# Kernel optimization log

Measured on AMD Instinct MI355X. Metric: run time of the kernel, lower is better.

Reference implementation:

```python
import jax, jax.numpy as jnp
import numpy as np

B, T, C = 4, 2048, 1024
H = 16  # NUM_HEADS
HD = C // H  # head_dim = 64


def setup_inputs() -> dict:
    key = jax.random.key(0)
    k1, k2, k3 = jax.random.split(key, 3)
    x = jax.random.normal(k1, (B, T, C), dtype=jnp.float32)
    # nn.Linear weights: stored as [out, in]; apply as x @ W.T
    W_attn = jax.random.normal(k2, (3 * C, C), dtype=jnp.float32) * (1.0 / np.sqrt(C))
    W_proj = jax.random.normal(k3, (C, C), dtype=jnp.float32) * (1.0 / np.sqrt(C))
    return {"x": x, "W_attn": W_attn, "W_proj": W_proj}


def reference(x, W_attn, W_proj):
    Bv, Tv, Cv = x.shape
    qkv = x @ W_attn.T  # [B, T, 3C]
    q, k, v = jnp.split(qkv, 3, axis=2)
    # [B, H, T, HD]
    q = q.reshape(Bv, Tv, H, HD).transpose(0, 2, 1, 3)
    k = k.reshape(Bv, Tv, H, HD).transpose(0, 2, 1, 3)
    v = v.reshape(Bv, Tv, H, HD).transpose(0, 2, 1, 3)
    att = jnp.einsum("bhqd,bhkd->bhqk", q, k) * (1.0 / np.sqrt(HD))
    causal = jnp.tril(jnp.ones((Tv, Tv), dtype=bool))
    att = jnp.where(causal[None, None, :, :], att, -jnp.inf)
    att = jax.nn.softmax(att, axis=-1)
    y = jnp.einsum("bhqk,bhkd->bhqd", att, v)
    y = y.transpose(0, 2, 1, 3).reshape(Bv, Tv, Cv)
    return y @ W_proj.T
```

## Files before the change

kernel.cpp:

```cpp
#include <hip/hip_runtime.h>

typedef _Float16 f16;
typedef _Float16 half8 __attribute__((ext_vector_type(8)));
typedef _Float16 half4v __attribute__((ext_vector_type(4)));
typedef __fp16 fp16x2 __attribute__((ext_vector_type(2)));
typedef float floatx4 __attribute__((ext_vector_type(4)));
typedef unsigned int uint;

constexpr int Bsz = 4, Tseq = 2048, Cdim = 1024, NH = 16, HDim = 64;
constexpr int Mtok = Bsz * Tseq;
constexpr int NQT = Tseq / 64;
constexpr float QSCALE = 0.18033688f;

#define GLDS16(src, dst) __builtin_amdgcn_global_load_lds( \
    (const __attribute__((address_space(1))) void*)(src),  \
    (__attribute__((address_space(3))) void*)(dst), 16, 0, 0)

__device__ __forceinline__ float fexp2(float x) { return __builtin_amdgcn_exp2f(x); }
__device__ __forceinline__ uint pkrtz(float a, float b) {
  fp16x2 h = __builtin_amdgcn_cvt_pkrtz(a, b);
  return __builtin_bit_cast(uint, h);
}

__global__ void cvt3_kernel(const float* __restrict__ x, const float* __restrict__ wa,
                            const float* __restrict__ wp,
                            f16* __restrict__ xh, f16* __restrict__ wah, f16* __restrict__ wph) {
  constexpr int nx = Mtok * Cdim, nwa = 3 * Cdim * Cdim, nwp = Cdim * Cdim;
  int i = (blockIdx.x * blockDim.x + threadIdx.x) * 4;
  const float* src; f16* dst; int off;
  if (i < nx)            { src = x;  dst = xh;  off = i; }
  else if (i < nx + nwa) { src = wa; dst = wah; off = i - nx; }
  else                   { src = wp; dst = wph; off = i - nx - nwa; }
  float4 v = *(const float4*)(src + off);
  half4v o;
  o[0] = (f16)v.x; o[1] = (f16)v.y; o[2] = (f16)v.z; o[3] = (f16)v.w;
  *(half4v*)(dst + off) = o;
}

template<int EPI>
__device__ __forceinline__ void gemm_body(f16* As, f16* Bs,
    const f16* __restrict__ X, const f16* __restrict__ W,
    float* __restrict__ outF,
    f16* __restrict__ q_out, f16* __restrict__ k_out, f16* __restrict__ v_out,
    int N, int K, int bid)
{
  constexpr int BK = 32;
  const int tid = threadIdx.x;
  const int wave = tid >> 6;
  const int lane = tid & 63;
  const int g = lane >> 4, lm = lane & 15;
  const int nbn = N / 128;
  const int bm = bid / nbn;
  const int bn = bid % nbn;
  const int m0 = bm * 128, n0 = bn * 128;
  const int wr = wave >> 1, wc = wave & 1;

  floatx4 acc[4][4];
#pragma unroll
  for (int i = 0; i < 4; ++i)
#pragma unroll
    for (int j = 0; j < 4; ++j) acc[i][j] = (floatx4)0.0f;

  for (int k0 = 0; k0 < K; k0 += BK) {
    __syncthreads();
#pragma unroll
    for (int t = 0; t < 2; ++t) {
      int row = (wave * 2 + t) * 16 + (lane >> 2);
      int cg = (lane & 3) ^ ((row >> 1) & 3);
      const f16* srcA = X + (size_t)(m0 + row) * K + k0 + cg * 8;
      GLDS16(srcA, (char*)As + (wave * 2 + t) * 1024);
      const f16* srcB = W + (size_t)(n0 + row) * K + k0 + cg * 8;
      GLDS16(srcB, (char*)Bs + (wave * 2 + t) * 1024);
    }
    __syncthreads();

    half8 af[4], bf[4];
#pragma unroll
    for (int i = 0; i < 4; ++i) {
      int rowa = wr * 64 + i * 16 + lm;
      int cga = g ^ ((rowa >> 1) & 3);
      af[i] = *(const half8*)((const char*)As + rowa * 64 + cga * 16);
      int rowb = wc * 64 + i * 16 + lm;
      int cgb = g ^ ((rowb >> 1) & 3);
      bf[i] = *(const half8*)((const char*)Bs + rowb * 64 + cgb * 16);
    }
#pragma unroll
    for (int i = 0; i < 4; ++i)
#pragma unroll
      for (int j = 0; j < 4; ++j)
        acc[i][j] = __builtin_amdgcn_mfma_f32_16x16x32_f16(af[i], bf[j], acc[i][j], 0, 0, 0);
  }

#pragma unroll
  for (int i = 0; i < 4; ++i) {
#pragma unroll
    for (int j = 0; j < 4; ++j) {
#pragma unroll
      for (int r = 0; r < 4; ++r) {
        int m = m0 + wr * 64 + i * 16 + 4 * g + r;
        int n = n0 + wc * 64 + j * 16 + lm;
        float v = acc[i][j][r];
        if constexpr (EPI == 1) {
          outF[(size_t)m * N + n] = v;
        } else if constexpr (EPI == 0) {
          int which = n >> 10;
          int inner = n & 1023;
          int h = inner >> 6, hd = inner & 63;
          int b = m >> 11, t = m & 2047;
          if (which == 0) {
            v *= QSCALE;
            q_out[(((size_t)(b * NH + h)) * Tseq + t) * HDim + hd] = (f16)v;
          } else {
            k_out[(((size_t)(b * NH + h)) * Tseq + t) * HDim + hd] = (f16)v;
          }
        } else {
          int h = m >> 6, hd = m & 63;
          int b = n >> 11, t = n & 2047;
          v_out[(((size_t)(b * NH + h)) * HDim + hd) * Tseq + t] = (f16)v;
        }
      }
    }
  }
}

__global__ __launch_bounds__(256)
void qkv_kernel(const f16* __restrict__ xh, const f16* __restrict__ wAh,
                f16* __restrict__ Qh, f16* __restrict__ Kh, f16* __restrict__ Vth) {
  __shared__ __align__(16) f16 As[128 * 32];
  __shared__ __align__(16) f16 Bs[128 * 32];
  int sbid = (blockIdx.x & 7) * 192 + (blockIdx.x >> 3);
  if (sbid < 1024)
    gemm_body<0>(As, Bs, xh, wAh, nullptr, Qh, Kh, nullptr, 2048, Cdim, sbid);
  else
    gemm_body<2>(As, Bs, wAh + (size_t)2048 * Cdim, xh, nullptr, nullptr, nullptr, Vth,
                 Mtok, Cdim, sbid - 1024);
}

__global__ __launch_bounds__(256)
void proj_kernel(const f16* __restrict__ yh, const f16* __restrict__ wPh, float* __restrict__ out) {
  __shared__ __align__(16) f16 As[128 * 32];
  __shared__ __align__(16) f16 Bs[128 * 32];
  int sbid = (blockIdx.x & 7) * 64 + (blockIdx.x >> 3);
  gemm_body<1>(As, Bs, yh, wPh, out, nullptr, nullptr, nullptr, Cdim, Cdim, sbid);
}

__device__ __forceinline__ void softmax_tile(floatx4* s, float& l_run,
                                             bool diag, int j0, int qg, char* pwrow, int g, int lm) {
  if (diag) {
#pragma unroll
    for (int nf = 0; nf < 4; ++nf)
#pragma unroll
      for (int r = 0; r < 4; ++r)
        if (j0 + nf * 16 + 4 * g + r > qg) s[nf][r] = -1e30f;
  }
  float rs = 0.f;
#pragma unroll
  for (int nf = 0; nf < 4; ++nf) {
    float p0 = fexp2(s[nf][0]), p1 = fexp2(s[nf][1]);
    float p2 = fexp2(s[nf][2]), p3 = fexp2(s[nf][3]);
    rs += (p0 + p1) + (p2 + p3);
    uint lo = pkrtz(p0, p1), hi = pkrtz(p2, p3);
    int slot = 2 * nf + (g >> 1);
    uint2 u; u.x = lo; u.y = hi;
    *(uint2*)(pwrow + 16 * (slot ^ (lm & 7)) + 8 * (g & 1)) = u;
  }
  l_run += rs;
}

__device__ __forceinline__ void store_o(const floatx4* acc, float l, int q0w, int g, int lm,
                                        f16* __restrict__ Y, int b, int h) {
  l += __shfl_xor(l, 16, 64);
  l += __shfl_xor(l, 32, 64);
#pragma unroll
  for (int r = 0; r < 4; ++r) {
    float lq = __shfl(l, 4 * g + r, 64);
    float inv = 1.0f / lq;
    int t = q0w + 4 * g + r;
    size_t base = ((size_t)(b * Tseq + t)) * Cdim + h * HDim;
#pragma unroll
    for (int ng = 0; ng < 4; ++ng)
      Y[base + ng * 16 + lm] = (f16)(acc[ng][r] * inv);
  }
}

__global__ __launch_bounds__(256)
void attn_kernel(const f16* __restrict__ Q, const f16* __restrict__ Kg,
                 const f16* __restrict__ Vt, f16* __restrict__ Y)
{
  __shared__ __align__(16) char smem[40960];
  int wg = blockIdx.x;
  int lin = (wg & 7) * 128 + (wg >> 3);
  const int p  = lin & 15;
  const int bh = lin >> 4;
  const int itB = NQT - p;
  const f16* Qb  = Q  + (size_t)bh * Tseq * HDim;
  const f16* Kb  = Kg + (size_t)bh * Tseq * HDim;
  const f16* Vtb = Vt + (size_t)bh * HDim * Tseq;

  const int tid = threadIdx.x, w = tid >> 6, lane = tid & 63;
  const int g = lane >> 4, lm = lane & 15;
  char* pwrow = smem + 32768 + w * 2048 + lm * 128;
  const int b = bh >> 4, h = bh & 15;

  int q0 = (NQT - 1 - p) * 64;
  int qg = q0 + w * 16 + lm;
  half8 qf0 = *(const half8*)(Qb + (size_t)(q0 + w * 16 + lm) * HDim + g * 8);
  half8 qf1 = *(const half8*)(Qb + (size_t)(q0 + w * 16 + lm) * HDim + 32 + g * 8);

  floatx4 acc[4];
  float l = 0.f;
#pragma unroll
  for (int ng = 0; ng < 4; ++ng) acc[ng] = (floatx4)0.f;

  const int srow = w * 8 + (lane >> 3);
  const int sslot = lane & 7;

  auto stage = [&](int j0s, int buf) {
#pragma unroll
    for (int t = 0; t < 2; ++t) {
      int row = srow + t * 32;
      int cg = sslot ^ (row & 7);
      GLDS16(Kb + (size_t)(j0s + row) * HDim + cg * 8,
             smem + buf * 8192 + (w * 8 + t * 32) * 128);
      GLDS16(Vtb + (size_t)row * Tseq + j0s + cg * 8,
             smem + 16384 + buf * 8192 + (w * 8 + t * 32) * 128);
    }
  };

  stage(0, 0);

  for (int it = 0; it < NQT + 1; ++it) {
    const bool lastB = (it == itB - 1);
    const bool last  = (it == NQT);
    const int jt = (it < itB) ? it : it - itB;
    const int j0 = jt * 64;

    if (!last) {
      const int itn = it + 1;
      const int jtn = (itn < itB) ? itn : itn - itB;
      stage(jtn * 64, itn & 1);
      asm volatile("s_waitcnt vmcnt(4)" ::: "memory");
    } else {
      asm volatile("s_waitcnt vmcnt(0)" ::: "memory");
    }
    __builtin_amdgcn_s_barrier();

    char* kb   = smem + (it & 1) * 8192;
    char* vbuf = smem + 16384 + (it & 1) * 8192;

    floatx4 s[4];
    __builtin_amdgcn_s_setprio(1);
#pragma unroll
    for (int nf = 0; nf < 4; ++nf) {
      half8 kf0 = *(const half8*)(kb + (nf * 16 + lm) * 128 + 16 * ((g)     ^ (lm & 7)));
      half8 kf1 = *(const half8*)(kb + (nf * 16 + lm) * 128 + 16 * ((4 + g) ^ (lm & 7)));
      s[nf] = __builtin_amdgcn_mfma_f32_16x16x32_f16(kf0, qf0, (floatx4)0.f, 0, 0, 0);
      s[nf] = __builtin_amdgcn_mfma_f32_16x16x32_f16(kf1, qf1, s[nf], 0, 0, 0);
    }
    __builtin_amdgcn_s_setprio(0);

    softmax_tile(s, l, lastB || last, j0, qg, pwrow, g, lm);
    half8 pa0 = *(const half8*)(pwrow + 16 * ((g)     ^ (lm & 7)));
    half8 pa1 = *(const half8*)(pwrow + 16 * ((4 + g) ^ (lm & 7)));

    __builtin_amdgcn_s_setprio(1);
#pragma unroll
    for (int c = 0; c < 2; ++c)
#pragma unroll
      for (int ng = 0; ng < 4; ++ng) {
        half8 vbf = *(const half8*)(vbuf + (ng * 16 + lm) * 128 + 16 * ((4 * c + g) ^ (lm & 7)));
        acc[ng] = __builtin_amdgcn_mfma_f32_16x16x32_f16(c ? pa1 : pa0, vbf, acc[ng], 0, 0, 0);
      }
    __builtin_amdgcn_s_setprio(0);

    __builtin_amdgcn_s_barrier();

    if (lastB) {
      store_o(acc, l, q0 + 16 * w, g, lm, Y, b, h);
      q0 = p * 64;
      qg = q0 + w * 16 + lm;
      qf0 = *(const half8*)(Qb + (size_t)(q0 + w * 16 + lm) * HDim + g * 8);
      qf1 = *(const half8*)(Qb + (size_t)(q0 + w * 16 + lm) * HDim + 32 + g * 8);
      l = 0.f;
#pragma unroll
      for (int ng = 0; ng < 4; ++ng) acc[ng] = (floatx4)0.f;
    }
  }

  store_o(acc, l, q0 + 16 * w, g, lm, Y, b, h);
}

extern "C" void kernel_launch(void* const* d_in, const int* in_sizes, int n_in,
                              void* d_out, int out_size, void* d_ws, size_t ws_size,
                              hipStream_t stream)
{
  const float* x      = (const float*)d_in[0];
  const float* W_attn = (const float*)d_in[1];
  const float* W_proj = (const float*)d_in[2];
  float* out = (float*)d_out;

  char* ws = (char*)d_ws;
  f16* xh  = (f16*)(ws);
  f16* wAh = (f16*)(ws + (size_t)(16u << 20));
  f16* wPh = (f16*)(ws + (size_t)(22u << 20));
  f16* Qh  = (f16*)(ws + (size_t)(24u << 20));
  f16* Kh  = (f16*)(ws + (size_t)(40u << 20));
  f16* Vth = (f16*)(ws + (size_t)(56u << 20));
  f16* yh  = xh;

  constexpr int ntot = (Mtok * Cdim + 3 * Cdim * Cdim + Cdim * Cdim) / 4;
  cvt3_kernel<<<(ntot + 255) / 256, 256, 0, stream>>>(x, W_attn, W_proj, xh, wAh, wPh);

  qkv_kernel<<<dim3(1536), 256, 0, stream>>>(xh, wAh, Qh, Kh, Vth);

  attn_kernel<<<dim3(1024), 256, 0, stream>>>(Qh, Kh, Vth, yh);

  proj_kernel<<<dim3(512), 256, 0, stream>>>(yh, wPh, out);
}
```

Measured before the change: 172.3 us.

## Double-buffer LDS in GEMM body to overlap global loads with MFMA

The shared GEMM used by the QKV and projection kernels now uses two LDS stages. The loads for the next K slice are issued before the MFMAs on the current slice run, and fine-grained vmcnt waits replace the full syncthreads pair. This hides global-to-LDS latency behind compute in both GEMMs. In exchange, LDS per block doubles to 32 KB, which can lower occupancy, and correctness now relies on hand-written waitcnt and barrier ordering.

```diff
diff --git a/kernel.cpp b/kernel.cpp
--- a/kernel.cpp
+++ b/kernel.cpp
@@ -38,7 +38,7 @@
 }
 
 template<int EPI>
-__device__ __forceinline__ void gemm_body(f16* As, f16* Bs,
+__device__ __forceinline__ void gemm_body(char* smem,
     const f16* __restrict__ X, const f16* __restrict__ W,
     float* __restrict__ outF,
     f16* __restrict__ q_out, f16* __restrict__ k_out, f16* __restrict__ v_out,
@@ -55,40 +55,61 @@
   const int m0 = bm * 128, n0 = bn * 128;
   const int wr = wave >> 1, wc = wave & 1;
 
+  const int srow = (lane >> 2);
+  const int scg0 = (lane & 3);
+
+  auto stageAB = [&](int k0, int buf) {
+#pragma unroll
+    for (int t = 0; t < 2; ++t) {
+      int row = (wave * 2 + t) * 16 + srow;
+      int cg = scg0 ^ ((row >> 1) & 3);
+      GLDS16(X + (size_t)(m0 + row) * K + k0 + cg * 8,
+             smem + buf * 16384 + (wave * 2 + t) * 1024);
+      GLDS16(W + (size_t)(n0 + row) * K + k0 + cg * 8,
+             smem + buf * 16384 + 8192 + (wave * 2 + t) * 1024);
+    }
+  };
+
   floatx4 acc[4][4];
 #pragma unroll
   for (int i = 0; i < 4; ++i)
 #pragma unroll
     for (int j = 0; j < 4; ++j) acc[i][j] = (floatx4)0.0f;
 
+  stageAB(0, 0);
+  int cur = 0;
+
   for (int k0 = 0; k0 < K; k0 += BK) {
-    __syncthreads();
-#pragma unroll
-    for (int t = 0; t < 2; ++t) {
-      int row = (wave * 2 + t) * 16 + (lane >> 2);
-      int cg = (lane & 3) ^ ((row >> 1) & 3);
-      const f16* srcA = X + (size_t)(m0 + row) * K + k0 + cg * 8;
-      GLDS16(srcA, (char*)As + (wave * 2 + t) * 1024);
-      const f16* srcB = W + (size_t)(n0 + row) * K + k0 + cg * 8;
-      GLDS16(srcB, (char*)Bs + (wave * 2 + t) * 1024);
-    }
-    __syncthreads();
+    const bool more = (k0 + BK < K);
+    if (more) {
+      stageAB(k0 + BK, cur ^ 1);
+      asm volatile("s_waitcnt vmcnt(4)" ::: "memory");
+    } else {
+      asm volatile("s_waitcnt vmcnt(0)" ::: "memory");
+    }
+    __builtin_amdgcn_s_barrier();
+
+    const char* As = smem + cur * 16384;
+    const char* Bs = smem + cur * 16384 + 8192;
 
     half8 af[4], bf[4];
 #pragma unroll
     for (int i = 0; i < 4; ++i) {
       int rowa = wr * 64 + i * 16 + lm;
       int cga = g ^ ((rowa >> 1) & 3);
-      af[i] = *(const half8*)((const char*)As + rowa * 64 + cga * 16);
+      af[i] = *(const half8*)(As + rowa * 64 + cga * 16);
       int rowb = wc * 64 + i * 16 + lm;
       int cgb = g ^ ((rowb >> 1) & 3);
-      bf[i] = *(const half8*)((const char*)Bs + rowb * 64 + cgb * 16);
+      bf[i] = *(const half8*)(Bs + rowb * 64 + cgb * 16);
     }
 #pragma unroll
     for (int i = 0; i < 4; ++i)
 #pragma unroll
       for (int j = 0; j < 4; ++j)
         acc[i][j] = __builtin_amdgcn_mfma_f32_16x16x32_f16(af[i], bf[j], acc[i][j], 0, 0, 0);
+
+    __builtin_amdgcn_s_barrier();
+    cur ^= 1;
   }
 
 #pragma unroll
@@ -126,22 +147,20 @@
 __global__ __launch_bounds__(256)
 void qkv_kernel(const f16* __restrict__ xh, const f16* __restrict__ wAh,
                 f16* __restrict__ Qh, f16* __restrict__ Kh, f16* __restrict__ Vth) {
-  __shared__ __align__(16) f16 As[128 * 32];
-  __shared__ __align__(16) f16 Bs[128 * 32];
+  __shared__ __align__(16) char smem[32768];
   int sbid = (blockIdx.x & 7) * 192 + (blockIdx.x >> 3);
   if (sbid < 1024)
-    gemm_body<0>(As, Bs, xh, wAh, nullptr, Qh, Kh, nullptr, 2048, Cdim, sbid);
+    gemm_body<0>(smem, xh, wAh, nullptr, Qh, Kh, nullptr, 2048, Cdim, sbid);
   else
-    gemm_body<2>(As, Bs, wAh + (size_t)2048 * Cdim, xh, nullptr, nullptr, nullptr, Vth,
+    gemm_body<2>(smem, wAh + (size_t)2048 * Cdim, xh, nullptr, nullptr, nullptr, Vth,
                  Mtok, Cdim, sbid - 1024);
 }
 
 __global__ __launch_bounds__(256)
 void proj_kernel(const f16* __restrict__ yh, const f16* __restrict__ wPh, float* __restrict__ out) {
-  __shared__ __align__(16) f16 As[128 * 32];
-  __shared__ __align__(16) f16 Bs[128 * 32];
+  __shared__ __align__(16) char smem[32768];
   int sbid = (blockIdx.x & 7) * 64 + (blockIdx.x >> 3);
-  gemm_body<1>(As, Bs, yh, wPh, out, nullptr, nullptr, nullptr, Cdim, Cdim, sbid);
+  gemm_body<1>(smem, yh, wPh, out, nullptr, nullptr, nullptr, Cdim, Cdim, sbid);
 }
 
 __device__ __forceinline__ void softmax_tile(floatx4* s, float& l_run,
```

New measurement: 178.0 us. 1.03x slower.

## Fuse x fp32-to-fp16 conversion into QKV GEMM tile loads

Applied to the files above, without the earlier changes.

The standalone conversion of activation x to fp16 is removed. The QKV GEMM now loads fp32 x tiles directly into LDS with a new XOR swizzle and converts them to half8 when reading fragments, so the fp16 copy of x is never written to or read back from global memory. The cost is twice the LDS footprint for the x operand and twice the global bytes per x tile inside the GEMM, which is re-read across the N tiles, plus extra conversion ALU work in the inner loop.

```diff
diff --git a/kernel.cpp b/kernel.cpp
--- a/kernel.cpp
+++ b/kernel.cpp
@@ -22,29 +22,28 @@
   return __builtin_bit_cast(uint, h);
 }
 
-__global__ void cvt3_kernel(const float* __restrict__ x, const float* __restrict__ wa,
-                            const float* __restrict__ wp,
-                            f16* __restrict__ xh, f16* __restrict__ wah, f16* __restrict__ wph) {
-  constexpr int nx = Mtok * Cdim, nwa = 3 * Cdim * Cdim, nwp = Cdim * Cdim;
+__global__ void cvt2_kernel(const float* __restrict__ wa, const float* __restrict__ wp,
+                            f16* __restrict__ wah, f16* __restrict__ wph) {
+  constexpr int nwa = 3 * Cdim * Cdim;
   int i = (blockIdx.x * blockDim.x + threadIdx.x) * 4;
   const float* src; f16* dst; int off;
-  if (i < nx)            { src = x;  dst = xh;  off = i; }
-  else if (i < nx + nwa) { src = wa; dst = wah; off = i - nx; }
-  else                   { src = wp; dst = wph; off = i - nx - nwa; }
+  if (i < nwa) { src = wa; dst = wah; off = i; }
+  else         { src = wp; dst = wph; off = i - nwa; }
   float4 v = *(const float4*)(src + off);
   half4v o;
   o[0] = (f16)v.x; o[1] = (f16)v.y; o[2] = (f16)v.z; o[3] = (f16)v.w;
   *(half4v*)(dst + off) = o;
 }
 
-template<int EPI>
-__device__ __forceinline__ void gemm_body(f16* As, f16* Bs,
-    const f16* __restrict__ X, const f16* __restrict__ W,
+template<int EPI, int AF32, int BF32>
+__device__ __forceinline__ void gemm_body(char* smem,
+    const void* Aop, const void* Bop,
     float* __restrict__ outF,
     f16* __restrict__ q_out, f16* __restrict__ k_out, f16* __restrict__ v_out,
     int N, int K, int bid)
 {
   constexpr int BK = 32;
+  constexpr int BOFF = AF32 ? 16384 : 8192;
   const int tid = threadIdx.x;
   const int wave = tid >> 6;
   const int lane = tid & 63;
@@ -63,14 +62,43 @@
 
   for (int k0 = 0; k0 < K; k0 += BK) {
     __syncthreads();
-#pragma unroll
-    for (int t = 0; t < 2; ++t) {
-      int row = (wave * 2 + t) * 16 + (lane >> 2);
-      int cg = (lane & 3) ^ ((row >> 1) & 3);
-      const f16* srcA = X + (size_t)(m0 + row) * K + k0 + cg * 8;
-      GLDS16(srcA, (char*)As + (wave * 2 + t) * 1024);
-      const f16* srcB = W + (size_t)(n0 + row) * K + k0 + cg * 8;
-      GLDS16(srcB, (char*)Bs + (wave * 2 + t) * 1024);
+    if constexpr (AF32) {
+      const float* Af = (const float*)Aop;
+#pragma unroll
+      for (int t = 0; t < 4; ++t) {
+        int row = wave * 8 + (lane >> 3) + t * 32;
+        int s = (lane & 7) ^ (row & 7);
+        GLDS16(Af + (size_t)(m0 + row) * K + k0 + s * 4,
+               smem + (wave * 8 + t * 32) * 128);
+      }
+    } else {
+      const f16* Ah = (const f16*)Aop;
+#pragma unroll
+      for (int t = 0; t < 2; ++t) {
+        int row = (wave * 2 + t) * 16 + (lane >> 2);
+        int cg = (lane & 3) ^ ((row >> 1) & 3);
+        GLDS16(Ah + (size_t)(m0 + row) * K + k0 + cg * 8,
+               smem + (wave * 2 + t) * 1024);
+      }
+    }
+    if constexpr (BF32) {
+      const float* Bf = (const float*)Bop;
+#pragma unroll
+      for (int t = 0; t < 4; ++t) {
+        int row = wave * 8 + (lane >> 3) + t * 32;
+        int s = (lane & 7) ^ (row & 7);
+        GLDS16(Bf + (size_t)(n0 + row) * K + k0 + s * 4,
+               smem + BOFF + (wave * 8 + t * 32) * 128);
+      }
+    } else {
+      const f16* Bh = (const f16*)Bop;
+#pragma unroll
+      for (int t = 0; t < 2; ++t) {
+        int row = (wave * 2 + t) * 16 + (lane >> 2);
+        int cg = (lane & 3) ^ ((row >> 1) & 3);
+        GLDS16(Bh + (size_t)(n0 + row) * K + k0 + cg * 8,
+               smem + BOFF + (wave * 2 + t) * 1024);
+      }
     }
     __syncthreads();
 
@@ -78,11 +106,29 @@
 #pragma unroll
     for (int i = 0; i < 4; ++i) {
       int rowa = wr * 64 + i * 16 + lm;
-      int cga = g ^ ((rowa >> 1) & 3);
-      af[i] = *(const half8*)((const char*)As + rowa * 64 + cga * 16);
+      if constexpr (AF32) {
+        float4 f0 = *(const float4*)(smem + rowa * 128 + 16 * ((2 * g)     ^ (rowa & 7)));
+        float4 f1 = *(const float4*)(smem + rowa * 128 + 16 * ((2 * g + 1) ^ (rowa & 7)));
+        half8 v;
+        v[0] = (f16)f0.x; v[1] = (f16)f0.y; v[2] = (f16)f0.z; v[3] = (f16)f0.w;
+        v[4] = (f16)f1.x; v[5] = (f16)f1.y; v[6] = (f16)f1.z; v[7] = (f16)f1.w;
+        af[i] = v;
+      } else {
+        int cga = g ^ ((rowa >> 1) & 3);
+        af[i] = *(const half8*)(smem + rowa * 64 + cga * 16);
+      }
       int rowb = wc * 64 + i * 16 + lm;
-      int cgb = g ^ ((rowb >> 1) & 3);
-      bf[i] = *(const half8*)((const char*)Bs + rowb * 64 + cgb * 16);
+      if constexpr (BF32) {
+        float4 f0 = *(const float4*)(smem + BOFF + rowb * 128 + 16 * ((2 * g)     ^ (rowb & 7)));
+        float4 f1 = *(const float4*)(smem + BOFF + rowb * 128 + 16 * ((2 * g + 1) ^ (rowb & 7)));
+        half8 v;
+        v[0] = (f16)f0.x; v[1] = (f16)f0.y; v[2] = (f16)f0.z; v[3] = (f16)f0.w;
+        v[4] = (f16)f1.x; v[5] = (f16)f1.y; v[6] = (f16)f1.z; v[7] = (f16)f1.w;
+        bf[i] = v;
+      } else {
+        int cgb = g ^ ((rowb >> 1) & 3);
+        bf[i] = *(const half8*)(smem + BOFF + rowb * 64 + cgb * 16);
+      }
     }
 #pragma unroll
     for (int i = 0; i < 4; ++i)
@@ -124,24 +170,22 @@
 }
 
 __global__ __launch_bounds__(256)
-void qkv_kernel(const f16* __restrict__ xh, const f16* __restrict__ wAh,
+void qkv_kernel(const float* __restrict__ x, const f16* __restrict__ wAh,
                 f16* __restrict__ Qh, f16* __restrict__ Kh, f16* __restrict__ Vth) {
-  __shared__ __align__(16) f16 As[128 * 32];
-  __shared__ __align__(16) f16 Bs[128 * 32];
+  __shared__ __align__(16) char smem[24576];
   int sbid = (blockIdx.x & 7) * 192 + (blockIdx.x >> 3);
   if (sbid < 1024)
-    gemm_body<0>(As, Bs, xh, wAh, nullptr, Qh, Kh, nullptr, 2048, Cdim, sbid);
+    gemm_body<0, 1, 0>(smem, x, wAh, nullptr, Qh, Kh, nullptr, 2048, Cdim, sbid);
   else
-    gemm_body<2>(As, Bs, wAh + (size_t)2048 * Cdim, xh, nullptr, nullptr, nullptr, Vth,
-                 Mtok, Cdim, sbid - 1024);
+    gemm_body<2, 0, 1>(smem, wAh + (size_t)2048 * Cdim, x, nullptr, nullptr, nullptr, Vth,
+                       Mtok, Cdim, sbid - 1024);
 }
 
 __global__ __launch_bounds__(256)
 void proj_kernel(const f16* __restrict__ yh, const f16* __restrict__ wPh, float* __restrict__ out) {
-  __shared__ __align__(16) f16 As[128 * 32];
-  __shared__ __align__(16) f16 Bs[128 * 32];
+  __shared__ __align__(16) char smem[16384];
   int sbid = (blockIdx.x & 7) * 64 + (blockIdx.x >> 3);
-  gemm_body<1>(As, Bs, yh, wPh, out, nullptr, nullptr, nullptr, Cdim, Cdim, sbid);
+  gemm_body<1, 0, 0>(smem, yh, wPh, out, nullptr, nullptr, nullptr, Cdim, Cdim, sbid);
 }
 
 __device__ __forceinline__ void softmax_tile(floatx4* s, float& l_run,
@@ -300,18 +344,17 @@
   float* out = (float*)d_out;
 
   char* ws = (char*)d_ws;
-  f16* xh  = (f16*)(ws);
-  f16* wAh = (f16*)(ws + (size_t)(16u << 20));
-  f16* wPh = (f16*)(ws + (size_t)(22u << 20));
-  f16* Qh  = (f16*)(ws + (size_t)(24u << 20));
-  f16* Kh  = (f16*)(ws + (size_t)(40u << 20));
-  f16* Vth = (f16*)(ws + (size_t)(56u << 20));
-  f16* yh  = xh;
-
-  constexpr int ntot = (Mtok * Cdim + 3 * Cdim * Cdim + Cdim * Cdim) / 4;
-  cvt3_kernel<<<(ntot + 255) / 256, 256, 0, stream>>>(x, W_attn, W_proj, xh, wAh, wPh);
-
-  qkv_kernel<<<dim3(1536), 256, 0, stream>>>(xh, wAh, Qh, Kh, Vth);
+  f16* wAh = (f16*)(ws);
+  f16* wPh = (f16*)(ws + (size_t)(6u << 20));
+  f16* Qh  = (f16*)(ws + (size_t)(8u << 20));
+  f16* Kh  = (f16*)(ws + (size_t)(24u << 20));
+  f16* Vth = (f16*)(ws + (size_t)(40u << 20));
+  f16* yh  = (f16*)(ws + (size_t)(56u << 20));
+
+  constexpr int ntot = (3 * Cdim * Cdim + Cdim * Cdim) / 4;
+  cvt2_kernel<<<ntot / 256, 256, 0, stream>>>(W_attn, W_proj, wAh, wPh);
+
+  qkv_kernel<<<dim3(1536), 256, 0, stream>>>(x, wAh, Qh, Kh, Vth);
 
   attn_kernel<<<dim3(1024), 256, 0, stream>>>(Qh, Kh, Vth, yh);
 
```

After: 194.0 us. 12.6% more time.
